# Performance work log

Measured on AMD Instinct MI355X. Metric: run time of the kernel, lower is better.

Reference implementation:

```python
import jax, jax.numpy as jnp
import numpy as np


def setup_inputs() -> dict:
    key = jax.random.key(0)
    k1, k2, k3, k4, k5 = jax.random.split(key, 5)
    B, C, H, W = 8, 512, 64, 64
    mid = C // 8
    x = jax.random.normal(k1, (B, C, H, W), dtype=jnp.float32)
    # 1x1 convs (no bias) are just channel-mixing matrices
    Wb = jax.random.normal(k2, (mid, C), dtype=jnp.float32) * (1.0 / np.sqrt(C))
    Wc = jax.random.normal(k3, (mid, C), dtype=jnp.float32) * (1.0 / np.sqrt(C))
    Wd = jax.random.normal(k4, (C, C), dtype=jnp.float32) * (1.0 / np.sqrt(C))
    gamma = jax.random.normal(k5, (1,), dtype=jnp.float32)
    return {"x": x, "Wb": Wb, "Wc": Wc, "Wd": Wd, "gamma": gamma}


def reference(x, Wb, Wc, Wd, gamma):
    B, C, H, W = x.shape
    N = H * W
    xf = x.reshape(B, C, N)                          # (B, C, N)
    b = jnp.einsum('mc,bcn->bnm', Wb, xf)            # queries  (B, N, mid)
    c = jnp.einsum('mc,bcn->bmn', Wc, xf)            # keys     (B, mid, N)
    d = jnp.einsum('oc,bcn->bno', Wd, xf)            # values   (B, N, C)
    # unscaled scores, softmax over keys (last dim), as in the source
    attn = jax.nn.softmax(jnp.einsum('bnm,bmk->bnk', b, c), axis=-1)  # (B, N, N)
    out = jnp.einsum('bnk,bko->bno', attn, d)        # (B, N, C)
    out = out.transpose(0, 2, 1).reshape(B, C, H, W)
    return gamma * out + x
```

## Files before the change

### kernel.cpp

```cpp
#include <hip/hip_runtime.h>

typedef unsigned short u16;
typedef _Float16 f16x8 __attribute__((ext_vector_type(8)));
typedef short bf16x8 __attribute__((ext_vector_type(8)));
typedef float f32x16 __attribute__((ext_vector_type(16)));
typedef unsigned int u32x4 __attribute__((ext_vector_type(4)));
typedef unsigned int u32x2 __attribute__((ext_vector_type(2)));

#define LOG2E 1.44269504088896340736f

static __device__ __forceinline__ u16 f2h(float f){
  union { _Float16 h; u16 u; } v; v.h = (_Float16)f; return v.u;
}
static __device__ __forceinline__ u16 f2bf(float f){
  union { float f; unsigned u; } v; v.f = f;
  return (u16)((v.u + 0x7fffu + ((v.u >> 16) & 1u)) >> 16);
}
static __device__ __forceinline__ unsigned pk2bf(float lo, float hi){
  unsigned r; asm("v_cvt_pk_bf16_f32 %0, %1, %2" : "=v"(r) : "v"(lo), "v"(hi)); return r;
}
static __device__ __forceinline__ float ex2(float x){
#if __has_builtin(__builtin_amdgcn_exp2f)
  return __builtin_amdgcn_exp2f(x);
#else
  return exp2f(x);
#endif
}
#define PSWAP(a, b) asm("v_permlane32_swap_b32 %0, %1" : "+v"(a), "+v"(b))

__global__ __launch_bounds__(256) void k_tr(const float* __restrict__ x, u16* __restrict__ xt){
  int bx = blockIdx.x;
  int nb = bx & 63, cb = (bx >> 6) & 7, b = bx >> 9;
  __shared__ u16 lt[64 * 68];
  int t = threadIdx.x;
  int cl = t >> 4, n0 = (t & 15) * 4;
  const float* xp = x + ((size_t)(b * 512 + cb * 64)) * 4096 + nb * 64;
#pragma unroll
  for (int i = 0; i < 4; ++i) {
    int c = cl + i * 16;
    float4 v = *(const float4*)(xp + (size_t)c * 4096 + n0);
    u16* d = &lt[c * 68 + n0];
    d[0] = f2h(v.x); d[1] = f2h(v.y); d[2] = f2h(v.z); d[3] = f2h(v.w);
  }
  __syncthreads();
  u16* xo = xt + ((size_t)(b * 4096 + nb * 64)) * 512 + cb * 64;
#pragma unroll
  for (int i = 0; i < 2; ++i) {
    int s = t + i * 256;
    int n = s >> 3, ch = s & 7;
    u32x4 o;
#pragma unroll
    for (int j = 0; j < 4; ++j) {
      u16 a = lt[(ch * 8 + 2 * j) * 68 + n];
      u16 bb = lt[(ch * 8 + 2 * j + 1) * 68 + n];
      o[j] = (unsigned)a | ((unsigned)bb << 16);
    }
    *(u32x4*)(xo + (size_t)n * 512 + ch * 8) = o;
  }
}

__global__ __launch_bounds__(512) void k_pqk(const u16* __restrict__ xt, const float* __restrict__ wb,
                                             const float* __restrict__ wc, u16* __restrict__ qk){
  int bx = blockIdx.x;
  int nb = bx & 31, b = bx >> 5;
  __shared__ u16 lx[128 * 64];
  __shared__ u16 lw[128 * 64];
  int t = threadIdx.x, w = t >> 6, l = t & 63, hi = l >> 5, ln = l & 31;
  int wr = w >> 1, wcol = w & 1;
  f32x16 acc[2] = {};
  for (int kt = 0; kt < 8; ++kt) {
    int c0 = kt * 64;
#pragma unroll
    for (int i = 0; i < 2; ++i) {
      int s = t + i * 512; int row = s >> 3, ch = s & 7;
      u32x4 v = *(const u32x4*)(xt + ((size_t)(b * 4096 + nb * 128 + row)) * 512 + c0 + ch * 8);
      *(u32x4*)((char*)lx + ((row * 128 + ch * 16) ^ ((row & 7) << 4))) = v;
    }
#pragma unroll
    for (int i = 0; i < 4; ++i) {
      int s = t + i * 512; int row = s >> 4, c4 = s & 15;
      const float* src = (row < 64) ? (wb + (size_t)row * 512 + c0 + c4 * 4)
                                    : (wc + (size_t)(row - 64) * 512 + c0 + c4 * 4);
      float4 v = *(const float4*)src;
      float sc = (row < 64) ? LOG2E : 1.0f;
      unsigned lo = (unsigned)f2h(v.x * sc) | ((unsigned)f2h(v.y * sc) << 16);
      unsigned h2 = (unsigned)f2h(v.z * sc) | ((unsigned)f2h(v.w * sc) << 16);
      unsigned long long qv = ((unsigned long long)h2 << 32) | lo;
      *(unsigned long long*)((char*)lw + ((row * 128 + c4 * 8) ^ ((row & 7) << 4))) = qv;
    }
    __syncthreads();
#pragma unroll
    for (int cc = 0; cc < 4; ++cc) {
      int ra = wr * 32 + ln;
      f16x8 a = *(const f16x8*)((char*)lx + ((ra * 128 + cc * 32 + hi * 16) ^ ((ra & 7) << 4)));
#pragma unroll
      for (int mt = 0; mt < 2; ++mt) {
        int rb = wcol * 64 + mt * 32 + ln;
        f16x8 bb = *(const f16x8*)((char*)lw + ((rb * 128 + cc * 32 + hi * 16) ^ ((rb & 7) << 4)));
        acc[mt] = __builtin_amdgcn_mfma_f32_32x32x16_f16(a, bb, acc[mt], 0, 0, 0);
      }
    }
    __syncthreads();
  }
#pragma unroll
  for (int mt = 0; mt < 2; ++mt)
#pragma unroll
    for (int r = 0; r < 16; ++r) {
      int n = wr * 32 + (r & 3) + 8 * (r >> 2) + 4 * hi;
      int m = wcol * 64 + mt * 32 + ln;
      qk[((size_t)(b * 4096 + nb * 128 + n)) * 128 + m] = f2h(acc[mt][r]);
    }
}

__global__ __launch_bounds__(512) void k_pv(const u16* __restrict__ xt, const float* __restrict__ wd,
                                            u16* __restrict__ vt){
  int bx = blockIdx.x;
  int nb = bx & 31, ob = (bx >> 5) & 3, b = bx >> 7;
  __shared__ u16 lx[128 * 64];
  __shared__ u16 lw[128 * 64];
  int t = threadIdx.x, w = t >> 6, l = t & 63, hi = l >> 5, ln = l & 31;
  int wr = w >> 2, wn = w & 3;
  f32x16 acc[2] = {};
  for (int kt = 0; kt < 8; ++kt) {
    int c0 = kt * 64;
#pragma unroll
    for (int i = 0; i < 2; ++i) {
      int s = t + i * 512; int row = s >> 3, ch = s & 7;
      u32x4 v = *(const u32x4*)(xt + ((size_t)(b * 4096 + nb * 128 + row)) * 512 + c0 + ch * 8);
      *(u32x4*)((char*)lx + ((row * 128 + ch * 16) ^ ((row & 7) << 4))) = v;
    }
#pragma unroll
    for (int i = 0; i < 4; ++i) {
      int s = t + i * 512; int row = s >> 4, c4 = s & 15;
      const float* src = wd + (size_t)(ob * 128 + row) * 512 + c0 + c4 * 4;
      float4 v = *(const float4*)src;
      unsigned lo = (unsigned)f2h(v.x) | ((unsigned)f2h(v.y) << 16);
      unsigned h2 = (unsigned)f2h(v.z) | ((unsigned)f2h(v.w) << 16);
      unsigned long long qv = ((unsigned long long)h2 << 32) | lo;
      *(unsigned long long*)((char*)lw + ((row * 128 + c4 * 8) ^ ((row & 7) << 4))) = qv;
    }
    __syncthreads();
#pragma unroll
    for (int cc = 0; cc < 4; ++cc) {
      int rb = wn * 32 + ln;
      f16x8 bb = *(const f16x8*)((char*)lx + ((rb * 128 + cc * 32 + hi * 16) ^ ((rb & 7) << 4)));
#pragma unroll
      for (int ot = 0; ot < 2; ++ot) {
        int ra = wr * 64 + ot * 32 + ln;
        f16x8 a = *(const f16x8*)((char*)lw + ((ra * 128 + cc * 32 + hi * 16) ^ ((ra & 7) << 4)));
        acc[ot] = __builtin_amdgcn_mfma_f32_32x32x16_f16(a, bb, acc[ot], 0, 0, 0);
      }
    }
    __syncthreads();
  }
#pragma unroll
  for (int ot = 0; ot < 2; ++ot)
#pragma unroll
    for (int r = 0; r < 16; ++r) {
      int o = ob * 128 + wr * 64 + ot * 32 + (r & 3) + 8 * (r >> 2) + 4 * hi;
      int n = nb * 128 + wn * 32 + ln;
      vt[((size_t)(b * 512 + o)) * 4096 + n] = f2bf(acc[ot][r]);
    }
}

__global__ __launch_bounds__(512, 1) void k_attn2(const u16* __restrict__ qk, const u16* __restrict__ vt,
                                                  const float* __restrict__ x, const float* __restrict__ gamma,
                                                  float* __restrict__ out){
  __shared__ char smem[87040];
  int bx = blockIdx.x;
  int orig = (bx & 7) * 32 + (bx >> 3);
  int combo = orig >> 4, qt = orig & 15;
  int b = combo >> 1, oc2 = combo & 1;
  int obase = oc2 * 256;
  int t = threadIdx.x, w = t >> 6, l = t & 63, hi = l >> 5, ln = l & 31;
  int q = qt * 256 + w * 32 + ln;
  size_t b4096 = (size_t)b * 4096;
  f16x8 qf[4];
  {
    const u16* qrow = qk + (b4096 + q) * 128;
#pragma unroll
    for (int ch = 0; ch < 4; ++ch) qf[ch] = *(const f16x8*)(qrow + ch * 16 + hi * 8);
  }
  int rowS = t >> 3, chS = t & 7;
  unsigned w8 = (unsigned)(rowS * 17 + chS * 2);
  unsigned rb8[4];
#pragma unroll
  for (int cc = 0; cc < 4; ++cc)
    rb8[cc] = (unsigned)(ln * 17 + cc * 4 + hi * 2);
  const u16* gK = qk + (b4096 + rowS) * 128 + 64 + chS * 8;
  const u16* gV0 = vt + ((size_t)(b * 512 + obase + rowS)) * 4096 + chS * 8;
  const u16* gV1 = gV0 + (size_t)64 * 4096;
  const u16* gV2 = gV0 + (size_t)128 * 4096;
  const u16* gV3 = gV0 + (size_t)192 * 4096;
  u32x4 kreg = *(const u32x4*)gK;
  u32x4 vr0 = *(const u32x4*)gV0, vr1 = *(const u32x4*)gV1;
  u32x4 vr2 = *(const u32x4*)gV2, vr3 = *(const u32x4*)gV3;
  {
    char* bp = smem;
    *(u32x2*)(bp + w8 * 8)              = u32x2{kreg[0], kreg[1]};
    *(u32x2*)(bp + w8 * 8 + 8)          = u32x2{kreg[2], kreg[3]};
    *(u32x2*)(bp + 8704  + w8 * 8)      = u32x2{vr0[0], vr0[1]};
    *(u32x2*)(bp + 8704  + w8 * 8 + 8)  = u32x2{vr0[2], vr0[3]};
    *(u32x2*)(bp + 17408 + w8 * 8)      = u32x2{vr1[0], vr1[1]};
    *(u32x2*)(bp + 17408 + w8 * 8 + 8)  = u32x2{vr1[2], vr1[3]};
    *(u32x2*)(bp + 26112 + w8 * 8)      = u32x2{vr2[0], vr2[1]};
    *(u32x2*)(bp + 26112 + w8 * 8 + 8)  = u32x2{vr2[2], vr2[3]};
    *(u32x2*)(bp + 34816 + w8 * 8)      = u32x2{vr3[0], vr3[1]};
    *(u32x2*)(bp + 34816 + w8 * 8 + 8)  = u32x2{vr3[2], vr3[3]};
  }
  gK += 8192; gV0 += 64; gV1 += 64; gV2 += 64; gV3 += 64;
  f32x16 acc[8] = {};
  float lacc = 0.0f;
  for (int kt = 0; kt < 64; ++kt) {
    __syncthreads();
    char* bufp = smem + (kt & 1) * 43520;
    char* bufn = smem + ((kt + 1) & 1) * 43520;
    if (kt < 63) {
      kreg = *(const u32x4*)gK;
      vr0 = *(const u32x4*)gV0; vr1 = *(const u32x4*)gV1;
      vr2 = *(const u32x4*)gV2; vr3 = *(const u32x4*)gV3;
      gK += 8192; gV0 += 64; gV1 += 64; gV2 += 64; gV3 += 64;
    }
    f32x16 s0 = {}, s1 = {};
    __builtin_amdgcn_s_setprio(1);
#pragma unroll
    for (int cc = 0; cc < 4; ++cc) {
      union { u32x2 d[2]; f16x8 v; } k0, k1;
      const char* p0 = bufp + rb8[cc] * 8;
      const char* p1 = p0 + 4352;
      k0.d[0] = *(const u32x2*)p0;  k0.d[1] = *(const u32x2*)(p0 + 8);
      k1.d[0] = *(const u32x2*)p1;  k1.d[1] = *(const u32x2*)(p1 + 8);
      s0 = __builtin_amdgcn_mfma_f32_32x32x16_f16(k0.v, qf[cc], s0, 0, 0, 0);
      s1 = __builtin_amdgcn_mfma_f32_32x32x16_f16(k1.v, qf[cc], s1, 0, 0, 0);
    }
    __builtin_amdgcn_s_setprio(0);
    float psum = 0.0f;
#pragma unroll
    for (int blk = 0; blk < 4; ++blk) {
      f32x16& sv = (blk < 2) ? s0 : s1;
      const int base = (blk & 1) * 8;
      float e[8];
#pragma unroll
      for (int j = 0; j < 8; ++j) e[j] = ex2(sv[base + j]);
      psum += ((e[0] + e[1]) + (e[2] + e[3])) + ((e[4] + e[5]) + (e[6] + e[7]));
      unsigned c[4];
      c[0] = pk2bf(e[0], e[1]); c[1] = pk2bf(e[2], e[3]);
      c[2] = pk2bf(e[4], e[5]); c[3] = pk2bf(e[6], e[7]);
      PSWAP(c[0], c[2]); PSWAP(c[1], c[3]);
      union U8 { unsigned u[4]; bf16x8 v; } pa;
      pa.u[0] = c[0]; pa.u[1] = c[1]; pa.u[2] = c[2]; pa.u[3] = c[3];
      const char* pv = bufp + 8704 + rb8[blk] * 8;
      __builtin_amdgcn_s_setprio(1);
#pragma unroll
      for (int ot = 0; ot < 8; ++ot) {
        union { u32x2 d[2]; bf16x8 v; } vb;
        const char* p = pv + ot * 4352;
        vb.d[0] = *(const u32x2*)p;  vb.d[1] = *(const u32x2*)(p + 8);
        acc[ot] = __builtin_amdgcn_mfma_f32_32x32x16_bf16(pa.v, vb.v, acc[ot], 0, 0, 0);
      }
      __builtin_amdgcn_s_setprio(0);
    }
    lacc += psum;
    if (kt < 63) {
      *(u32x2*)(bufn + w8 * 8)              = u32x2{kreg[0], kreg[1]};
      *(u32x2*)(bufn + w8 * 8 + 8)          = u32x2{kreg[2], kreg[3]};
      *(u32x2*)(bufn + 8704  + w8 * 8)      = u32x2{vr0[0], vr0[1]};
      *(u32x2*)(bufn + 8704  + w8 * 8 + 8)  = u32x2{vr0[2], vr0[3]};
      *(u32x2*)(bufn + 17408 + w8 * 8)      = u32x2{vr1[0], vr1[1]};
      *(u32x2*)(bufn + 17408 + w8 * 8 + 8)  = u32x2{vr1[2], vr1[3]};
      *(u32x2*)(bufn + 26112 + w8 * 8)      = u32x2{vr2[0], vr2[1]};
      *(u32x2*)(bufn + 26112 + w8 * 8 + 8)  = u32x2{vr2[2], vr2[3]};
      *(u32x2*)(bufn + 34816 + w8 * 8)      = u32x2{vr3[0], vr3[1]};
      *(u32x2*)(bufn + 34816 + w8 * 8 + 8)  = u32x2{vr3[2], vr3[3]};
    }
  }
  float l_tot = lacc + __shfl_xor(lacc, 32);
  float sinv = gamma[0] / l_tot;
  __syncthreads();
  float* tb = (float*)smem + w * 1056;
#pragma unroll
  for (int ot = 0; ot < 8; ++ot) {
#pragma unroll
    for (int r = 0; r < 16; ++r) {
      int qr = (r & 3) + 8 * (r >> 2) + 4 * hi;
      tb[ln * 33 + qr] = acc[ot][r];
    }
#pragma unroll
    for (int it = 0; it < 16; ++it) {
      int orow = it * 2 + hi;
      float v = tb[orow * 33 + ln];
      size_t gi = (((size_t)(b * 512 + obase + ot * 32 + orow)) << 12) + (size_t)(qt * 256 + w * 32 + ln);
      out[gi] = sinv * v + x[gi];
    }
    __syncthreads();
  }
}

extern "C" void kernel_launch(void* const* d_in, const int* in_sizes, int n_in,
                              void* d_out, int out_size, void* d_ws, size_t ws_size,
                              hipStream_t stream) {
  (void)in_sizes; (void)n_in; (void)out_size; (void)ws_size;
  const float* x     = (const float*)d_in[0];
  const float* wb    = (const float*)d_in[1];
  const float* wc    = (const float*)d_in[2];
  const float* wd    = (const float*)d_in[3];
  const float* gamma = (const float*)d_in[4];
  float* out = (float*)d_out;
  char* ws = (char*)d_ws;
  u16* xt  = (u16*)ws;
  u16* qkb = (u16*)(ws + 33554432);
  u16* vtb = (u16*)(ws + 41943040);
  k_tr   <<<dim3(4096), dim3(256), 0, stream>>>(x, xt);
  k_pqk  <<<dim3(256),  dim3(512), 0, stream>>>(xt, wb, wc, qkb);
  k_pv   <<<dim3(1024), dim3(512), 0, stream>>>(xt, wd, vtb);
  k_attn2<<<dim3(256),  dim3(512), 0, stream>>>(qkb, vtb, x, gamma, out);
}
```

Measured before the change: 254.7 us.

## Halve attention block to 4 waves and 32-key tiles for two blocks per CU

The attention kernel now uses 256-thread blocks covering 128 queries, processes 32 keys per iteration instead of 64, and halves the shared-memory double buffer so two blocks can be resident per CU. The grid doubles to 512 blocks with a new block-to-tile mapping, and the K/V shared layouts are re-padded. The aim is better latency hiding through two co-resident blocks and fuller CU coverage. The cost is twice as many loop iterations and barriers, and each K/V tile is reloaded by twice as many blocks.

```diff
diff --git a/kernel.cpp b/kernel.cpp
--- a/kernel.cpp
+++ b/kernel.cpp
@@ -163,17 +163,16 @@
     }
 }
 
-__global__ __launch_bounds__(512, 1) void k_attn2(const u16* __restrict__ qk, const u16* __restrict__ vt,
+__global__ __launch_bounds__(256, 2) void k_attn2(const u16* __restrict__ qk, const u16* __restrict__ vt,
                                                   const float* __restrict__ x, const float* __restrict__ gamma,
                                                   float* __restrict__ out){
-  __shared__ char smem[87040];
+  __shared__ char smem[45568];
   int bx = blockIdx.x;
-  int orig = (bx & 7) * 32 + (bx >> 3);
-  int combo = orig >> 4, qt = orig & 15;
-  int b = combo >> 1, oc2 = combo & 1;
+  int orig = (bx & 7) * 64 + (bx >> 3);
+  int b = orig >> 6, oc2 = (orig >> 5) & 1, qt = orig & 31;
   int obase = oc2 * 256;
   int t = threadIdx.x, w = t >> 6, l = t & 63, hi = l >> 5, ln = l & 31;
-  int q = qt * 256 + w * 32 + ln;
+  int q = qt * 128 + w * 32 + ln;
   size_t b4096 = (size_t)b * 4096;
   f16x8 qf[4];
   {
@@ -181,14 +180,18 @@
 #pragma unroll
     for (int ch = 0; ch < 4; ++ch) qf[ch] = *(const f16x8*)(qrow + ch * 16 + hi * 8);
   }
-  int rowS = t >> 3, chS = t & 7;
-  unsigned w8 = (unsigned)(rowS * 17 + chS * 2);
-  unsigned rb8[4];
-#pragma unroll
-  for (int cc = 0; cc < 4; ++cc)
-    rb8[cc] = (unsigned)(ln * 17 + cc * 4 + hi * 2);
-  const u16* gK = qk + (b4096 + rowS) * 128 + 64 + chS * 8;
-  const u16* gV0 = vt + ((size_t)(b * 512 + obase + rowS)) * 4096 + chS * 8;
+  int rK = t >> 3, chK = t & 7;
+  int rV = t >> 2, ch4 = t & 3;
+  unsigned kW = (unsigned)(rK * 136 + chK * 16);
+  unsigned vW = (unsigned)(4352 + rV * 72 + ch4 * 16);
+  unsigned rbK[4];
+#pragma unroll
+  for (int cc = 0; cc < 4; ++cc) rbK[cc] = (unsigned)(ln * 136 + cc * 32 + hi * 16);
+  unsigned rbV[2];
+#pragma unroll
+  for (int kc = 0; kc < 2; ++kc) rbV[kc] = (unsigned)(4352 + ln * 72 + kc * 32 + hi * 16);
+  const u16* gK = qk + (b4096 + rK) * 128 + 64 + chK * 8;
+  const u16* gV0 = vt + ((size_t)(b * 512 + obase + rV)) * 4096 + ch4 * 8;
   const u16* gV1 = gV0 + (size_t)64 * 4096;
   const u16* gV2 = gV0 + (size_t)128 * 4096;
   const u16* gV3 = gV0 + (size_t)192 * 4096;
@@ -197,51 +200,47 @@
   u32x4 vr2 = *(const u32x4*)gV2, vr3 = *(const u32x4*)gV3;
   {
     char* bp = smem;
-    *(u32x2*)(bp + w8 * 8)              = u32x2{kreg[0], kreg[1]};
-    *(u32x2*)(bp + w8 * 8 + 8)          = u32x2{kreg[2], kreg[3]};
-    *(u32x2*)(bp + 8704  + w8 * 8)      = u32x2{vr0[0], vr0[1]};
-    *(u32x2*)(bp + 8704  + w8 * 8 + 8)  = u32x2{vr0[2], vr0[3]};
-    *(u32x2*)(bp + 17408 + w8 * 8)      = u32x2{vr1[0], vr1[1]};
-    *(u32x2*)(bp + 17408 + w8 * 8 + 8)  = u32x2{vr1[2], vr1[3]};
-    *(u32x2*)(bp + 26112 + w8 * 8)      = u32x2{vr2[0], vr2[1]};
-    *(u32x2*)(bp + 26112 + w8 * 8 + 8)  = u32x2{vr2[2], vr2[3]};
-    *(u32x2*)(bp + 34816 + w8 * 8)      = u32x2{vr3[0], vr3[1]};
-    *(u32x2*)(bp + 34816 + w8 * 8 + 8)  = u32x2{vr3[2], vr3[3]};
-  }
-  gK += 8192; gV0 += 64; gV1 += 64; gV2 += 64; gV3 += 64;
+    *(u32x2*)(bp + kW)              = u32x2{kreg[0], kreg[1]};
+    *(u32x2*)(bp + kW + 8)          = u32x2{kreg[2], kreg[3]};
+    *(u32x2*)(bp + vW)              = u32x2{vr0[0], vr0[1]};
+    *(u32x2*)(bp + vW + 8)          = u32x2{vr0[2], vr0[3]};
+    *(u32x2*)(bp + vW + 4608)       = u32x2{vr1[0], vr1[1]};
+    *(u32x2*)(bp + vW + 4616)       = u32x2{vr1[2], vr1[3]};
+    *(u32x2*)(bp + vW + 9216)       = u32x2{vr2[0], vr2[1]};
+    *(u32x2*)(bp + vW + 9224)       = u32x2{vr2[2], vr2[3]};
+    *(u32x2*)(bp + vW + 13824)      = u32x2{vr3[0], vr3[1]};
+    *(u32x2*)(bp + vW + 13832)      = u32x2{vr3[2], vr3[3]};
+  }
+  gK += 4096; gV0 += 32; gV1 += 32; gV2 += 32; gV3 += 32;
   f32x16 acc[8] = {};
   float lacc = 0.0f;
-  for (int kt = 0; kt < 64; ++kt) {
-    __syncthreads();
-    char* bufp = smem + (kt & 1) * 43520;
-    char* bufn = smem + ((kt + 1) & 1) * 43520;
-    if (kt < 63) {
+  for (int kt = 0; kt < 128; ++kt) {
+    __syncthreads();
+    char* bufp = smem + (kt & 1) * 22784;
+    char* bufn = smem + ((kt + 1) & 1) * 22784;
+    if (kt < 127) {
       kreg = *(const u32x4*)gK;
       vr0 = *(const u32x4*)gV0; vr1 = *(const u32x4*)gV1;
       vr2 = *(const u32x4*)gV2; vr3 = *(const u32x4*)gV3;
-      gK += 8192; gV0 += 64; gV1 += 64; gV2 += 64; gV3 += 64;
-    }
-    f32x16 s0 = {}, s1 = {};
+      gK += 4096; gV0 += 32; gV1 += 32; gV2 += 32; gV3 += 32;
+    }
+    f32x16 s0 = {};
     __builtin_amdgcn_s_setprio(1);
 #pragma unroll
     for (int cc = 0; cc < 4; ++cc) {
-      union { u32x2 d[2]; f16x8 v; } k0, k1;
-      const char* p0 = bufp + rb8[cc] * 8;
-      const char* p1 = p0 + 4352;
+      union { u32x2 d[2]; f16x8 v; } k0;
+      const char* p0 = bufp + rbK[cc];
       k0.d[0] = *(const u32x2*)p0;  k0.d[1] = *(const u32x2*)(p0 + 8);
-      k1.d[0] = *(const u32x2*)p1;  k1.d[1] = *(const u32x2*)(p1 + 8);
       s0 = __builtin_amdgcn_mfma_f32_32x32x16_f16(k0.v, qf[cc], s0, 0, 0, 0);
-      s1 = __builtin_amdgcn_mfma_f32_32x32x16_f16(k1.v, qf[cc], s1, 0, 0, 0);
     }
     __builtin_amdgcn_s_setprio(0);
     float psum = 0.0f;
 #pragma unroll
-    for (int blk = 0; blk < 4; ++blk) {
-      f32x16& sv = (blk < 2) ? s0 : s1;
-      const int base = (blk & 1) * 8;
+    for (int blk = 0; blk < 2; ++blk) {
+      const int base = blk * 8;
       float e[8];
 #pragma unroll
-      for (int j = 0; j < 8; ++j) e[j] = ex2(sv[base + j]);
+      for (int j = 0; j < 8; ++j) e[j] = ex2(s0[base + j]);
       psum += ((e[0] + e[1]) + (e[2] + e[3])) + ((e[4] + e[5]) + (e[6] + e[7]));
       unsigned c[4];
       c[0] = pk2bf(e[0], e[1]); c[1] = pk2bf(e[2], e[3]);
@@ -249,29 +248,29 @@
       PSWAP(c[0], c[2]); PSWAP(c[1], c[3]);
       union U8 { unsigned u[4]; bf16x8 v; } pa;
       pa.u[0] = c[0]; pa.u[1] = c[1]; pa.u[2] = c[2]; pa.u[3] = c[3];
-      const char* pv = bufp + 8704 + rb8[blk] * 8;
+      const char* pv = bufp + rbV[blk];
       __builtin_amdgcn_s_setprio(1);
 #pragma unroll
       for (int ot = 0; ot < 8; ++ot) {
         union { u32x2 d[2]; bf16x8 v; } vb;
-        const char* p = pv + ot * 4352;
+        const char* p = pv + ot * 2304;
         vb.d[0] = *(const u32x2*)p;  vb.d[1] = *(const u32x2*)(p + 8);
         acc[ot] = __builtin_amdgcn_mfma_f32_32x32x16_bf16(pa.v, vb.v, acc[ot], 0, 0, 0);
       }
       __builtin_amdgcn_s_setprio(0);
     }
     lacc += psum;
-    if (kt < 63) {
-      *(u32x2*)(bufn + w8 * 8)              = u32x2{kreg[0], kreg[1]};
-      *(u32x2*)(bufn + w8 * 8 + 8)          = u32x2{kreg[2], kreg[3]};
-      *(u32x2*)(bufn + 8704  + w8 * 8)      = u32x2{vr0[0], vr0[1]};
-      *(u32x2*)(bufn + 8704  + w8 * 8 + 8)  = u32x2{vr0[2], vr0[3]};
-      *(u32x2*)(bufn + 17408 + w8 * 8)      = u32x2{vr1[0], vr1[1]};
-      *(u32x2*)(bufn + 17408 + w8 * 8 + 8)  = u32x2{vr1[2], vr1[3]};
-      *(u32x2*)(bufn + 26112 + w8 * 8)      = u32x2{vr2[0], vr2[1]};
-      *(u32x2*)(bufn + 26112 + w8 * 8 + 8)  = u32x2{vr2[2], vr2[3]};
-      *(u32x2*)(bufn + 34816 + w8 * 8)      = u32x2{vr3[0], vr3[1]};
-      *(u32x2*)(bufn + 34816 + w8 * 8 + 8)  = u32x2{vr3[2], vr3[3]};
+    if (kt < 127) {
+      *(u32x2*)(bufn + kW)              = u32x2{kreg[0], kreg[1]};
+      *(u32x2*)(bufn + kW + 8)          = u32x2{kreg[2], kreg[3]};
+      *(u32x2*)(bufn + vW)              = u32x2{vr0[0], vr0[1]};
+      *(u32x2*)(bufn + vW + 8)          = u32x2{vr0[2], vr0[3]};
+      *(u32x2*)(bufn + vW + 4608)       = u32x2{vr1[0], vr1[1]};
+      *(u32x2*)(bufn + vW + 4616)       = u32x2{vr1[2], vr1[3]};
+      *(u32x2*)(bufn + vW + 9216)       = u32x2{vr2[0], vr2[1]};
+      *(u32x2*)(bufn + vW + 9224)       = u32x2{vr2[2], vr2[3]};
+      *(u32x2*)(bufn + vW + 13824)      = u32x2{vr3[0], vr3[1]};
+      *(u32x2*)(bufn + vW + 13832)      = u32x2{vr3[2], vr3[3]};
     }
   }
   float l_tot = lacc + __shfl_xor(lacc, 32);
@@ -289,7 +288,7 @@
     for (int it = 0; it < 16; ++it) {
       int orow = it * 2 + hi;
       float v = tb[orow * 33 + ln];
-      size_t gi = (((size_t)(b * 512 + obase + ot * 32 + orow)) << 12) + (size_t)(qt * 256 + w * 32 + ln);
+      size_t gi = (((size_t)(b * 512 + obase + ot * 32 + orow)) << 12) + (size_t)(qt * 128 + w * 32 + ln);
       out[gi] = sinv * v + x[gi];
     }
     __syncthreads();
@@ -313,5 +312,5 @@
   k_tr   <<<dim3(4096), dim3(256), 0, stream>>>(x, xt);
   k_pqk  <<<dim3(256),  dim3(512), 0, stream>>>(xt, wb, wc, qkb);
   k_pv   <<<dim3(1024), dim3(512), 0, stream>>>(xt, wd, vtb);
-  k_attn2<<<dim3(256),  dim3(512), 0, stream>>>(qkb, vtb, x, gamma, out);
-}
+  k_attn2<<<dim3(512),  dim3(256), 0, stream>>>(qkb, vtb, x, gamma, out);
+}
```

New measurement: 272.0 us. +6.8%, slower.
